# Kernel optimization log

Measured on AMD Instinct MI355X. Metric: run time of the kernel, lower is better.

The kernel has to match this reference:

```python
import jax, jax.numpy as jnp
import numpy as np


def squash(s, axis):
    # torch: mag_sq/(1+mag_sq) * s/mag, reduced over the given axis
    mag_sq = jnp.sum(s * s, axis=axis, keepdims=True)
    mag = jnp.sqrt(mag_sq)
    return mag_sq / (1.0 + mag_sq) * (s / mag)


def setup_inputs() -> dict:
    key = jax.random.key(0)
    ks = jax.random.split(key, 13)
    B, D_IN, H = 64, 227989, 512
    NU, CO, K = 8, 8, 8            # num_primary_units, conv out channels, kernel
    L = (H - K) // 2 + 1           # 253
    PSIZE = NU * 0 + CO * L        # 2024 per primary capsule
    NOUT, USIZE = 4, 64            # output capsules
    f32 = jnp.float32
    return {
        "x": jax.random.normal(ks[0], (B, D_IN), f32),
        "fc_w": jax.random.normal(ks[1], (H, D_IN), f32) * 0.002,
        "fc_b": jax.random.normal(ks[2], (H,), f32) * 0.01,
        "conv_w": jax.random.normal(ks[3], (NU, CO, 1, K), f32) * 0.1,
        "conv_b": jax.random.normal(ks[4], (NU, CO), f32) * 0.01,
        "W_dig": jax.random.normal(ks[5], (PSIZE, NOUT, USIZE, NU), f32) * 0.05,
        "fc2_w1": jax.random.normal(ks[6], (128, 256), f32) * 0.05,
        "fc2_b1": jnp.zeros((128,), f32),
        "fc2_w2": jax.random.normal(ks[7], (64, 128), f32) * 0.08,
        "fc2_b2": jnp.zeros((64,), f32),
        "fc2_w3": jax.random.normal(ks[8], (2, 64), f32) * 0.1,
        "fc2_b3": jnp.zeros((2,), f32),
    }


def reference(x, fc_w, fc_b, conv_w, conv_b, W_dig,
              fc2_w1, fc2_b1, fc2_w2, fc2_b2, fc2_w3, fc2_b3):
    B = x.shape[0]
    # fc + ReLU (nn.ReLU overwrote the LeakyReLU attribute)
    sdae = jnp.maximum(x @ fc_w.T + fc_b, 0.0)[:, None, :]   # [B,1,512]

    # primary capsules (no routing): 8 ConvUnits fused into one conv
    NU, CO, _, K = conv_w.shape
    rhs = conv_w.reshape(NU * CO, 1, K)
    u = jax.lax.conv_general_dilated(sdae, rhs, (2,), 'VALID',
                                     dimension_numbers=('NCH', 'OIH', 'NCH'))
    u = u + conv_b.reshape(1, NU * CO, 1)                     # [B,64,253]
    u = u.reshape(B, NU, -1)                                  # [B,8,2024]
    u = squash(u, 2)

    # digits capsule: dynamic routing, 3 iterations
    xt = jnp.swapaxes(u, 1, 2)                                # [B,2024,8]
    u_hat = jnp.einsum('cjdi,bci->bcjd', W_dig, xt)           # [B,2024,4,64]
    C, J = W_dig.shape[0], W_dig.shape[1]
    b_ij = jnp.zeros((C, J), u_hat.dtype)
    for _ in range(3):
        c_ij = jax.nn.softmax(b_ij, axis=0)                   # softmax over in_channels
        s_j = jnp.einsum('cj,bcjd->bjd', c_ij, u_hat)         # [B,4,64]
        v_j = squash(s_j, 1)                                  # torch squashes dim=2 = capsule dim j
        b_ij = b_ij + jnp.mean(jnp.einsum('bcjd,bjd->bcj', u_hat, v_j), axis=0)

    caps = v_j.reshape(B, -1)                                 # [B,256]
    lrelu = lambda z: jnp.where(z >= 0, z, 0.01 * z)          # LeakyReLU; dropout in eval = identity
    h = lrelu(caps @ fc2_w1.T + fc2_b1)
    h = lrelu(h @ fc2_w2.T + fc2_b2)
    logits = h @ fc2_w3.T + fc2_b3                            # [B,2]
    return (logits, sdae)
```

## Files before the change

kernel.cpp:

```cpp
#include <hip/hip_runtime.h>
#include <hip/hip_bf16.h>

typedef __attribute__((ext_vector_type(8))) short s16x8;
typedef __attribute__((ext_vector_type(4))) float f32x4;

#define D_IN 227989
#define KSPLIT 128
#define KC 1792
#define NSTEPS 28
#define RPITCH 68
#define BUFSZ (128 * RPITCH)

__device__ __forceinline__ s16x8 pk2(f32x4 lo, f32x4 hi) {
    union { int i[4]; s16x8 s; } u;
    asm("v_cvt_pk_bf16_f32 %0, %1, %2" : "=v"(u.i[0]) : "v"(lo[0]), "v"(lo[1]));
    asm("v_cvt_pk_bf16_f32 %0, %1, %2" : "=v"(u.i[1]) : "v"(lo[2]), "v"(lo[3]));
    asm("v_cvt_pk_bf16_f32 %0, %1, %2" : "=v"(u.i[2]) : "v"(hi[0]), "v"(hi[1]));
    asm("v_cvt_pk_bf16_f32 %0, %1, %2" : "=v"(u.i[3]) : "v"(hi[2]), "v"(hi[3]));
    return u.s;
}

__device__ __forceinline__ void gload_lds16(const float* g, float* l) {
    __builtin_amdgcn_global_load_lds(
        (const __attribute__((address_space(1))) void*)g,
        (__attribute__((address_space(3))) void*)l, 16, 0, 0);
}

__device__ __forceinline__ s16x8 sel8(const float* rowp, int pos0, bool b0, bool b1) {
    f32x4 i0 = *(const f32x4*)(rowp + pos0);
    f32x4 i1 = *(const f32x4*)(rowp + pos0 + 4);
    f32x4 i2 = *(const f32x4*)(rowp + pos0 + 8);
    float in[12] = {i0[0], i0[1], i0[2], i0[3], i1[0], i1[1], i1[2], i1[3],
                    i2[0], i2[1], i2[2], i2[3]};
    float tv[10];
    #pragma unroll
    for (int i = 0; i < 10; ++i) tv[i] = b0 ? in[i + 1] : in[i];
    f32x4 lo, hi;
    #pragma unroll
    for (int e = 0; e < 4; ++e) lo[e] = b1 ? tv[e + 2] : tv[e];
    #pragma unroll
    for (int e = 0; e < 4; ++e) hi[e] = b1 ? tv[e + 6] : tv[e + 4];
    return pk2(lo, hi);
}

__device__ __forceinline__ void compute_tile(const float* buf, int wid, int frow,
                                             int koct, bool b0, bool b1, f32x4* acc) {
    const float* B = buf + (64 + wid * 16 + frow) * RPITCH;
    const s16x8 bb0 = sel8(B, koct * 8, b0, b1);
    const s16x8 bb1 = sel8(B, 32 + koct * 8, b0, b1);
    #pragma unroll
    for (int m = 0; m < 4; ++m) {
        const float* A = buf + (m * 16 + frow) * RPITCH;
        const s16x8 a0 = sel8(A, koct * 8, b0, b1);
        const s16x8 a1 = sel8(A, 32 + koct * 8, b0, b1);
        acc[m] = __builtin_amdgcn_mfma_f32_16x16x32_bf16(a0, bb0, acc[m], 0, 0, 0);
        acc[m] = __builtin_amdgcn_mfma_f32_16x16x32_bf16(a1, bb1, acc[m], 0, 0, 0);
    }
}

__global__ __launch_bounds__(256) void k_fc_gemm(const float* __restrict__ x,
                                                 const float* __restrict__ w,
                                                 float* __restrict__ part) {
    __shared__ __align__(16) float lds[2 * BUFSZ];
    const int t = threadIdx.x;
    const int wid = t >> 6, lane = t & 63;
    const int frow = lane & 15, koct = lane >> 4;
    const int bx = blockIdx.x;
    const int nt = bx & 7, ks = bx >> 3;
    const long k0 = (long)ks * KC;
    const bool b0 = (frow & 1) != 0, b1 = (frow & 2) != 0;

    f32x4 acc[4] = {};

    if (ks < KSPLIT - 1) {
        const float* gp[9];
        int jdst[9];
        #pragma unroll
        for (int jj = 0; jj < 9; ++jj) {
            int j = jj * 4 + wid;
            if (j >= 34) j -= 34;
            jdst[jj] = j * 256;
            const int ch = j * 64 + lane;
            const int row = ch / 17;
            const int c = ch - row * 17;
            const float* base = (row < 64)
                ? (x + (long)row * D_IN)
                : (w + (long)(nt * 64 + (row - 64)) * D_IN);
            gp[jj] = base + (k0 - (row & 3)) + c * 4;
        }
        float* L0 = lds;
        float* L1 = lds + BUFSZ;

#define STAGE(BUF, OFF) do {                                   \
    _Pragma("unroll")                                          \
    for (int jj = 0; jj < 9; ++jj)                             \
        gload_lds16(gp[jj] + (OFF), (BUF) + jdst[jj]);         \
} while (0)

        STAGE(L0, 0);
        #pragma unroll 1
        for (int s = 0; s < NSTEPS; s += 2) {
            STAGE(L1, (s + 1) * 64);
            asm volatile("s_waitcnt vmcnt(9)" ::: "memory");
            __builtin_amdgcn_s_barrier();
            asm volatile("" ::: "memory");
            compute_tile(L0, wid, frow, koct, b0, b1, acc);
            asm volatile("s_waitcnt lgkmcnt(0)" ::: "memory");
            __builtin_amdgcn_s_barrier();
            if (s + 2 < NSTEPS) {
                STAGE(L0, (s + 2) * 64);
                asm volatile("s_waitcnt vmcnt(9)" ::: "memory");
            } else {
                asm volatile("s_waitcnt vmcnt(0)" ::: "memory");
            }
            __builtin_amdgcn_s_barrier();
            asm volatile("" ::: "memory");
            compute_tile(L1, wid, frow, koct, b0, b1, acc);
            asm volatile("s_waitcnt lgkmcnt(0)" ::: "memory");
            __builtin_amdgcn_s_barrier();
        }
#undef STAGE
    } else {
        const int rem = (int)(D_IN - k0);
        const int nst = (rem + 63) >> 6;
        const float* ga = x + (long)(wid * 16) * D_IN + k0 + lane;
        const float* gb = w + (long)(nt * 64 + wid * 16) * D_IN + k0 + lane;
        for (int s = 0; s < nst; ++s) {
            const int kk = s * 64 + lane;
            const bool ok = kk < rem;
            float va[16], vb[16];
            #pragma unroll
            for (int i = 0; i < 16; ++i) {
                va[i] = ok ? ga[(long)i * D_IN + s * 64] : 0.0f;
                vb[i] = ok ? gb[(long)i * D_IN + s * 64] : 0.0f;
            }
            __syncthreads();
            #pragma unroll
            for (int i = 0; i < 16; ++i) {
                lds[(wid * 16 + i) * RPITCH + lane] = va[i];
                lds[(64 + wid * 16 + i) * RPITCH + lane] = vb[i];
            }
            if (lane < 8) {
                const int rr = (lane & 3), half = lane >> 2;
                (void)rr; (void)half;
            }
            __syncthreads();
            compute_tile(lds, wid, frow, koct, false, false, acc);
            __syncthreads();
        }
    }

    const int g16 = nt * 4 + wid;
    float* __restrict__ po = part + ((long)(g16 * KSPLIT + ks) << 10);
    #pragma unroll
    for (int m = 0; m < 4; ++m)
        #pragma unroll
        for (int r = 0; r < 4; ++r)
            po[(m * 16 + koct * 4 + r) * 16 + frow] = acc[m][r];
}

__global__ __launch_bounds__(256) void k_fc_reduce(const float* __restrict__ part,
                                                   const float* __restrict__ bias,
                                                   float* __restrict__ sdae) {
    const int i = blockIdx.x * 256 + threadIdx.x;
    const int m = i >> 9, n = i & 511;
    const int nt = n >> 4, nl = n & 15;
    const float* p = part + ((long)nt * KSPLIT << 10) + m * 16 + nl;
    float s = 0.f;
    #pragma unroll 4
    for (int ks = 0; ks < KSPLIT; ++ks) s += p[(long)ks << 10];
    s += bias[n];
    sdae[i] = fmaxf(s, 0.0f);
}

__global__ __launch_bounds__(256) void k_conv_squash(const float* __restrict__ sdae,
                                                     const float* __restrict__ cw,
                                                     const float* __restrict__ cb,
                                                     float* __restrict__ xt) {
    __shared__ float row_s[512];
    __shared__ float us[64 * 253];
    __shared__ float part[256];
    __shared__ float scale_s[8];
    const int b = blockIdx.x, t = threadIdx.x;
    row_s[t] = sdae[b * 512 + t];
    row_s[t + 256] = sdae[b * 512 + t + 256];
    __syncthreads();
    const int ch = t >> 2, lq = t & 3;
    float wreg[8];
    #pragma unroll
    for (int k = 0; k < 8; ++k) wreg[k] = cw[ch * 8 + k];
    const float bias = cb[ch];
    const int l0 = lq * 64;
    const int l1 = (lq == 3) ? 253 : (l0 + 64);
    float ssq = 0.f;
    for (int l = l0; l < l1; ++l) {
        float v = bias;
        #pragma unroll
        for (int k = 0; k < 8; ++k) v += row_s[2 * l + k] * wreg[k];
        us[ch * 253 + l] = v;
        ssq += v * v;
    }
    part[t] = ssq;
    __syncthreads();
    if (t < 8) {
        float s = 0.f;
        for (int i = 0; i < 32; ++i) s += part[t * 32 + i];
        scale_s[t] = sqrtf(s) / (1.0f + s);
    }
    __syncthreads();
    const int nu = ch >> 3, co = ch & 7;
    const float sc = scale_s[nu];
    for (int l = l0; l < l1; ++l)
        xt[(long)b * 16192 + (long)(co * 253 + l) * 8 + nu] = us[ch * 253 + l] * sc;
}

template <int UNIFORM>
__global__ __launch_bounds__(256) void k_route_s(const float* __restrict__ W,
                                                 const float* __restrict__ xt,
                                                 const float* __restrict__ cij,
                                                 float* __restrict__ spart) {
    __shared__ __align__(16) float xs[64 * 132];
    __shared__ __align__(16) float wsh[16 * 768];
    const int bx = blockIdx.x;
    const int j = bx >> 6, cs = bx & 63;
    const int c0 = cs * 32;
    const int t = threadIdx.x;
    const int bg = t >> 4, dg = t & 15;
    float acc[4][4] = {};
    #pragma unroll 1
    for (int cc0 = 0; cc0 < 32; cc0 += 16) {
        {
            const int bb = t >> 2, p = t & 3;
            const float* src = xt + (long)bb * 16192 + (long)(c0 + cc0) * 8 + p * 32;
            float* dst = &xs[bb * 132 + p * 32];
            if (c0 + cc0 + 16 <= 2024) {
                #pragma unroll
                for (int e = 0; e < 32; e += 4) *(f32x4*)(dst + e) = *(const f32x4*)(src + e);
            } else {
                for (int e = 0; e < 32; ++e) {
                    int cidx = c0 + cc0 + ((p * 32 + e) >> 3);
                    dst[e] = (cidx < 2024) ? src[e] : 0.0f;
                }
            }
        }
        {
            const int ccs = t >> 4, dp = t & 15;
            const int c = c0 + cc0 + ccs;
            float* o = &wsh[ccs * 768 + dp * 48];
            if (c < 2024) {
                const float sc = UNIFORM ? (1.0f / 2024.0f) : cij[j * 2024 + c];
                const float* wsrc = W + (long)c * 2048 + j * 512 + dp * 32;
                #pragma unroll
                for (int dd = 0; dd < 4; ++dd) {
                    f32x4 w0 = *(const f32x4*)(wsrc + dd * 8);
                    f32x4 w1 = *(const f32x4*)(wsrc + dd * 8 + 4);
                    float* od = o + dd * 12;
                    od[0] = w0[0] * sc; od[1] = w0[1] * sc; od[2] = w0[2] * sc; od[3] = w0[3] * sc;
                    od[4] = w1[0] * sc; od[5] = w1[1] * sc; od[6] = w1[2] * sc; od[7] = w1[3] * sc;
                }
            } else {
                #pragma unroll
                for (int dd = 0; dd < 4; ++dd) {
                    float* od = o + dd * 12;
                    #pragma unroll
                    for (int e = 0; e < 8; ++e) od[e] = 0.0f;
                }
            }
        }
        __syncthreads();
        int ccN = 2024 - c0 - cc0;
        if (ccN > 16) ccN = 16;
        for (int cc = 0; cc < ccN; ++cc) {
            float xv[4][8], wv[4][8];
            #pragma unroll
            for (int bb = 0; bb < 4; ++bb) {
                *(f32x4*)&xv[bb][0] = *(const f32x4*)&xs[(bg * 4 + bb) * 132 + cc * 8];
                *(f32x4*)&xv[bb][4] = *(const f32x4*)&xs[(bg * 4 + bb) * 132 + cc * 8 + 4];
            }
            #pragma unroll
            for (int dd = 0; dd < 4; ++dd) {
                const int d = dg + dd * 16;
                *(f32x4*)&wv[dd][0] = *(const f32x4*)&wsh[cc * 768 + d * 12];
                *(f32x4*)&wv[dd][4] = *(const f32x4*)&wsh[cc * 768 + d * 12 + 4];
            }
            #pragma unroll
            for (int bb = 0; bb < 4; ++bb)
                #pragma unroll
                for (int dd = 0; dd < 4; ++dd)
                    #pragma unroll
                    for (int i = 0; i < 8; ++i)
                        acc[bb][dd] += xv[bb][i] * wv[dd][i];
        }
        __syncthreads();
    }
    float* sp = spart + ((long)bx << 12);
    #pragma unroll
    for (int bb = 0; bb < 4; ++bb)
        #pragma unroll
        for (int dd = 0; dd < 4; ++dd)
            sp[(bg * 4 + bb) * 64 + dg + dd * 16] = acc[bb][dd];
}

__global__ __launch_bounds__(256) void k_route_v(const float* __restrict__ spart,
                                                 float* __restrict__ v) {
    __shared__ float sj[256];
    const int b = blockIdx.x, t = threadIdx.x;
    const int d = t & 63;
    const int j = t >> 6;
    float s = 0.f;
    #pragma unroll 4
    for (int cs = 0; cs < 64; ++cs)
        s += spart[((long)(j * 64 + cs) << 12) + (b << 6) + d];
    sj[t] = s;
    __syncthreads();
    float msq = 0.f;
    #pragma unroll
    for (int q = 0; q < 4; ++q) { float z = sj[q * 64 + d]; msq += z * z; }
    v[(b << 8) + t] = s * (sqrtf(msq) / (1.0f + msq));
}

template <int ADD>
__global__ __launch_bounds__(256) void k_route_a(const float* __restrict__ W,
                                                 const float* __restrict__ xt,
                                                 const float* __restrict__ v,
                                                 float* __restrict__ bij) {
    __shared__ __align__(16) float xts[64 * 68];
    __shared__ __align__(16) float vts[4 * 4360];
    __shared__ float red[256];
    const int c0 = blockIdx.x * 8;
    const int t = threadIdx.x;
    for (int idx = t; idx < 16384; idx += 256) {
        int b = idx >> 8, r = idx & 255;
        vts[(r >> 6) * 4360 + (r & 63) * 68 + b] = v[idx];
    }
    for (int idx = t; idx < 4096; idx += 256) {
        int b = idx >> 6, r = idx & 63;
        xts[r * 68 + b] = xt[(long)b * 16192 + (long)c0 * 8 + r];
    }
    __syncthreads();
    const int cc = t >> 5, jj = (t >> 3) & 3, p = t & 7;
    float Wreg[8][8];
    const float* wb = W + (long)(c0 + cc) * 2048 + jj * 512;
    #pragma unroll
    for (int dd = 0; dd < 8; ++dd) {
        const int d = p + dd * 8;
        *(f32x4*)&Wreg[dd][0] = *(const f32x4*)(wb + d * 8);
        *(f32x4*)&Wreg[dd][4] = *(const f32x4*)(wb + d * 8 + 4);
    }
    float a0 = 0.f, a1 = 0.f, a2 = 0.f, a3 = 0.f;
    for (int b0 = 0; b0 < 64; b0 += 4) {
        float xq[8][4];
        #pragma unroll
        for (int i = 0; i < 8; ++i)
            *(f32x4*)&xq[i][0] = *(const f32x4*)&xts[(cc * 8 + i) * 68 + b0];
        #pragma unroll
        for (int dd = 0; dd < 8; ++dd) {
            const int d = p + dd * 8;
            f32x4 vq = *(const f32x4*)&vts[jj * 4360 + d * 68 + b0];
            float u0 = 0, u1 = 0, u2 = 0, u3 = 0;
            #pragma unroll
            for (int i = 0; i < 8; ++i) {
                const float wv = Wreg[dd][i];
                u0 += wv * xq[i][0]; u1 += wv * xq[i][1];
                u2 += wv * xq[i][2]; u3 += wv * xq[i][3];
            }
            a0 += u0 * vq[0]; a1 += u1 * vq[1]; a2 += u2 * vq[2]; a3 += u3 * vq[3];
        }
    }
    red[t] = a0 + a1 + a2 + a3;
    __syncthreads();
    if (p == 0) {
        float s = 0.f;
        #pragma unroll
        for (int q2 = 0; q2 < 8; ++q2) s += red[t + q2];
        s *= (1.0f / 64.0f);
        const int idx = (c0 + cc) * 4 + jj;
        bij[idx] = ADD ? (bij[idx] + s) : s;
    }
}

__global__ __launch_bounds__(256) void k_softmax(const float* __restrict__ bij,
                                                 float* __restrict__ cij) {
    __shared__ float red[256];
    const int j = blockIdx.x, t = threadIdx.x;
    float vals[8];
    float m = -1e30f;
    #pragma unroll
    for (int q = 0; q < 8; ++q) {
        const int c = q * 256 + t;
        const float z = (c < 2024) ? bij[c * 4 + j] : -1e30f;
        vals[q] = z;
        m = fmaxf(m, z);
    }
    red[t] = m;
    __syncthreads();
    for (int s = 128; s > 0; s >>= 1) {
        if (t < s) red[t] = fmaxf(red[t], red[t + s]);
        __syncthreads();
    }
    m = red[0];
    __syncthreads();
    float sum = 0.f;
    #pragma unroll
    for (int q = 0; q < 8; ++q) {
        const int c = q * 256 + t;
        const float e = (c < 2024) ? __expf(vals[q] - m) : 0.0f;
        vals[q] = e;
        sum += e;
    }
    red[t] = sum;
    __syncthreads();
    for (int s = 128; s > 0; s >>= 1) {
        if (t < s) red[t] += red[t + s];
        __syncthreads();
    }
    const float inv = 1.0f / red[0];
    #pragma unroll
    for (int q = 0; q < 8; ++q) {
        const int c = q * 256 + t;
        if (c < 2024) cij[j * 2024 + c] = vals[q] * inv;
    }
}

__global__ __launch_bounds__(256) void k_fc2(const float* __restrict__ v,
                                             const float* __restrict__ w1, const float* __restrict__ b1,
                                             const float* __restrict__ w2, const float* __restrict__ b2,
                                             const float* __restrict__ w3, const float* __restrict__ b3,
                                             float* __restrict__ logits) {
    __shared__ float caps[256], h1[128], h2[64];
    const int b = blockIdx.x, t = threadIdx.x;
    caps[t] = v[b * 256 + t];
    __syncthreads();
    if (t < 128) {
        float s = b1[t];
        const float* wr = w1 + t * 256;
        for (int k = 0; k < 256; ++k) s += wr[k] * caps[k];
        h1[t] = (s >= 0.f) ? s : 0.01f * s;
    }
    __syncthreads();
    if (t < 64) {
        float s = b2[t];
        const float* wr = w2 + t * 128;
        for (int k = 0; k < 128; ++k) s += wr[k] * h1[k];
        h2[t] = (s >= 0.f) ? s : 0.01f * s;
    }
    __syncthreads();
    if (t < 2) {
        float s = b3[t];
        const float* wr = w3 + t * 64;
        for (int k = 0; k < 64; ++k) s += wr[k] * h2[k];
        logits[b * 2 + t] = s;
    }
}

extern "C" void kernel_launch(void* const* d_in, const int* in_sizes, int n_in,
                              void* d_out, int out_size, void* d_ws, size_t ws_size,
                              hipStream_t stream) {
    const float* x      = (const float*)d_in[0];
    const float* fc_w   = (const float*)d_in[1];
    const float* fc_b   = (const float*)d_in[2];
    const float* conv_w = (const float*)d_in[3];
    const float* conv_b = (const float*)d_in[4];
    const float* W_dig  = (const float*)d_in[5];
    const float* w1 = (const float*)d_in[6];
    const float* b1 = (const float*)d_in[7];
    const float* w2 = (const float*)d_in[8];
    const float* b2 = (const float*)d_in[9];
    const float* w3 = (const float*)d_in[10];
    const float* b3 = (const float*)d_in[11];

    float* out    = (float*)d_out;
    float* logits = out;
    float* sdae   = out + 128;

    float* ws     = (float*)d_ws;
    float* ws_fc  = ws;
    float* ws_xt  = ws_fc + 4194304;
    float* ws_sp  = ws_xt + 1036288;
    float* ws_v   = ws_sp + 1048576;
    float* ws_bij = ws_v + 16384;
    float* ws_cij = ws_bij + 8096;

    k_fc_gemm<<<1024, 256, 0, stream>>>(x, fc_w, ws_fc);
    k_fc_reduce<<<128, 256, 0, stream>>>(ws_fc, fc_b, sdae);
    k_conv_squash<<<64, 256, 0, stream>>>(sdae, conv_w, conv_b, ws_xt);

    k_route_s<1><<<256, 256, 0, stream>>>(W_dig, ws_xt, ws_cij, ws_sp);
    k_route_v<<<64, 256, 0, stream>>>(ws_sp, ws_v);
    k_route_a<0><<<253, 256, 0, stream>>>(W_dig, ws_xt, ws_v, ws_bij);
    k_softmax<<<4, 256, 0, stream>>>(ws_bij, ws_cij);
    k_route_s<0><<<256, 256, 0, stream>>>(W_dig, ws_xt, ws_cij, ws_sp);
    k_route_v<<<64, 256, 0, stream>>>(ws_sp, ws_v);
    k_route_a<1><<<253, 256, 0, stream>>>(W_dig, ws_xt, ws_v, ws_bij);
    k_softmax<<<4, 256, 0, stream>>>(ws_bij, ws_cij);
    k_route_s<0><<<256, 256, 0, stream>>>(W_dig, ws_xt, ws_cij, ws_sp);
    k_route_v<<<64, 256, 0, stream>>>(ws_sp, ws_v);

    k_fc2<<<64, 256, 0, stream>>>(ws_v, w1, b1, w2, b2, w3, b3, logits);
}
```

Before: 305.2 us.

## Double GEMM K-step per stage and fuse reduce/conv, softmax and final route kernels

The FC GEMM now stages 128 K-columns per LDS buffer instead of 64, halving the number of steps and barriers at the cost of twice the LDS footprint. The split-K reduction is fused into the conv+squash kernel, the softmax kernels are folded into route_s (each block recomputes the softmax reduction), and the last route_v is fused with the fc2 MLP. This removes four to five kernel launches and the c_ij round trip through memory, in exchange for redundant softmax work in every route_s block and lower occupancy in the GEMM from the larger shared buffers.

```diff
diff --git a/kernel.cpp b/kernel.cpp
--- a/kernel.cpp
+++ b/kernel.cpp
@@ -7,8 +7,8 @@
 #define D_IN 227989
 #define KSPLIT 128
 #define KC 1792
-#define NSTEPS 28
-#define RPITCH 68
+#define NSTEPS 14
+#define RPITCH 132
 #define BUFSZ (128 * RPITCH)
 
 __device__ __forceinline__ s16x8 pk2(f32x4 lo, f32x4 hi) {
@@ -43,18 +43,19 @@
     return pk2(lo, hi);
 }
 
-__device__ __forceinline__ void compute_tile(const float* buf, int wid, int frow,
-                                             int koct, bool b0, bool b1, f32x4* acc) {
+__device__ __forceinline__ void compute_tile128(const float* buf, int wid, int frow,
+                                                int koct, bool b0, bool b1, f32x4* acc) {
     const float* B = buf + (64 + wid * 16 + frow) * RPITCH;
-    const s16x8 bb0 = sel8(B, koct * 8, b0, b1);
-    const s16x8 bb1 = sel8(B, 32 + koct * 8, b0, b1);
-    #pragma unroll
-    for (int m = 0; m < 4; ++m) {
-        const float* A = buf + (m * 16 + frow) * RPITCH;
-        const s16x8 a0 = sel8(A, koct * 8, b0, b1);
-        const s16x8 a1 = sel8(A, 32 + koct * 8, b0, b1);
-        acc[m] = __builtin_amdgcn_mfma_f32_16x16x32_bf16(a0, bb0, acc[m], 0, 0, 0);
-        acc[m] = __builtin_amdgcn_mfma_f32_16x16x32_bf16(a1, bb1, acc[m], 0, 0, 0);
+    #pragma unroll
+    for (int kk = 0; kk < 4; ++kk) {
+        const int pos0 = kk * 32 + koct * 8;
+        const s16x8 bb = sel8(B, pos0, b0, b1);
+        #pragma unroll
+        for (int m = 0; m < 4; ++m) {
+            const float* A = buf + (m * 16 + frow) * RPITCH;
+            const s16x8 aa = sel8(A, pos0, b0, b1);
+            acc[m] = __builtin_amdgcn_mfma_f32_16x16x32_bf16(aa, bb, acc[m], 0, 0, 0);
+        }
     }
 }
 
@@ -73,49 +74,48 @@
     f32x4 acc[4] = {};
 
     if (ks < KSPLIT - 1) {
-        const float* gp[9];
-        int jdst[9];
-        #pragma unroll
-        for (int jj = 0; jj < 9; ++jj) {
-            int j = jj * 4 + wid;
-            if (j >= 34) j -= 34;
-            jdst[jj] = j * 256;
-            const int ch = j * 64 + lane;
-            const int row = ch / 17;
-            const int c = ch - row * 17;
+        const int wbase = (wid == 0) ? 0 : (wid == 1) ? 1088 : (wid == 2) ? 2176 : 3136;
+        const float* gp[17];
+        int jdst[17];
+        #pragma unroll
+        for (int jj = 0; jj < 17; ++jj) {
+            const int ch = wbase + jj * 64 + lane;
+            const int row = ch / 33;
+            const int c = ch - row * 33;
             const float* base = (row < 64)
                 ? (x + (long)row * D_IN)
                 : (w + (long)(nt * 64 + (row - 64)) * D_IN);
             gp[jj] = base + (k0 - (row & 3)) + c * 4;
+            jdst[jj] = (wbase + jj * 64) * 4;
         }
         float* L0 = lds;
         float* L1 = lds + BUFSZ;
 
 #define STAGE(BUF, OFF) do {                                   \
     _Pragma("unroll")                                          \
-    for (int jj = 0; jj < 9; ++jj)                             \
+    for (int jj = 0; jj < 17; ++jj)                            \
         gload_lds16(gp[jj] + (OFF), (BUF) + jdst[jj]);         \
 } while (0)
 
         STAGE(L0, 0);
         #pragma unroll 1
         for (int s = 0; s < NSTEPS; s += 2) {
-            STAGE(L1, (s + 1) * 64);
-            asm volatile("s_waitcnt vmcnt(9)" ::: "memory");
+            STAGE(L1, (s + 1) * 128);
+            asm volatile("s_waitcnt vmcnt(17)" ::: "memory");
             __builtin_amdgcn_s_barrier();
             asm volatile("" ::: "memory");
-            compute_tile(L0, wid, frow, koct, b0, b1, acc);
+            compute_tile128(L0, wid, frow, koct, b0, b1, acc);
             asm volatile("s_waitcnt lgkmcnt(0)" ::: "memory");
             __builtin_amdgcn_s_barrier();
             if (s + 2 < NSTEPS) {
-                STAGE(L0, (s + 2) * 64);
-                asm volatile("s_waitcnt vmcnt(9)" ::: "memory");
+                STAGE(L0, (s + 2) * 128);
+                asm volatile("s_waitcnt vmcnt(17)" ::: "memory");
             } else {
                 asm volatile("s_waitcnt vmcnt(0)" ::: "memory");
             }
             __builtin_amdgcn_s_barrier();
             asm volatile("" ::: "memory");
-            compute_tile(L1, wid, frow, koct, b0, b1, acc);
+            compute_tile128(L1, wid, frow, koct, b0, b1, acc);
             asm volatile("s_waitcnt lgkmcnt(0)" ::: "memory");
             __builtin_amdgcn_s_barrier();
         }
@@ -140,12 +140,19 @@
                 lds[(wid * 16 + i) * RPITCH + lane] = va[i];
                 lds[(64 + wid * 16 + i) * RPITCH + lane] = vb[i];
             }
-            if (lane < 8) {
-                const int rr = (lane & 3), half = lane >> 2;
-                (void)rr; (void)half;
-            }
             __syncthreads();
-            compute_tile(lds, wid, frow, koct, false, false, acc);
+            const float* B = lds + (64 + wid * 16 + frow) * RPITCH;
+            #pragma unroll
+            for (int q = 0; q < 2; ++q) {
+                const int pos0 = q * 32 + koct * 8;
+                const s16x8 bb = sel8(B, pos0, false, false);
+                #pragma unroll
+                for (int m = 0; m < 4; ++m) {
+                    const float* A = lds + (m * 16 + frow) * RPITCH;
+                    const s16x8 aa = sel8(A, pos0, false, false);
+                    acc[m] = __builtin_amdgcn_mfma_f32_16x16x32_bf16(aa, bb, acc[m], 0, 0, 0);
+                }
+            }
             __syncthreads();
         }
     }
@@ -159,31 +166,30 @@
             po[(m * 16 + koct * 4 + r) * 16 + frow] = acc[m][r];
 }
 
-__global__ __launch_bounds__(256) void k_fc_reduce(const float* __restrict__ part,
-                                                   const float* __restrict__ bias,
-                                                   float* __restrict__ sdae) {
-    const int i = blockIdx.x * 256 + threadIdx.x;
-    const int m = i >> 9, n = i & 511;
-    const int nt = n >> 4, nl = n & 15;
-    const float* p = part + ((long)nt * KSPLIT << 10) + m * 16 + nl;
-    float s = 0.f;
-    #pragma unroll 4
-    for (int ks = 0; ks < KSPLIT; ++ks) s += p[(long)ks << 10];
-    s += bias[n];
-    sdae[i] = fmaxf(s, 0.0f);
-}
-
-__global__ __launch_bounds__(256) void k_conv_squash(const float* __restrict__ sdae,
+__global__ __launch_bounds__(256) void k_reduce_conv(const float* __restrict__ part,
+                                                     const float* __restrict__ fc_b,
                                                      const float* __restrict__ cw,
                                                      const float* __restrict__ cb,
+                                                     float* __restrict__ sdae,
                                                      float* __restrict__ xt) {
     __shared__ float row_s[512];
     __shared__ float us[64 * 253];
-    __shared__ float part[256];
+    __shared__ float psum[256];
     __shared__ float scale_s[8];
     const int b = blockIdx.x, t = threadIdx.x;
-    row_s[t] = sdae[b * 512 + t];
-    row_s[t + 256] = sdae[b * 512 + t + 256];
+    #pragma unroll
+    for (int h = 0; h < 2; ++h) {
+        const int n = t + h * 256;
+        const int g16 = n >> 4, nl = n & 15;
+        const float* p = part + ((long)(g16 * KSPLIT) << 10) + b * 16 + nl;
+        float s = 0.f;
+        #pragma unroll 4
+        for (int ks = 0; ks < KSPLIT; ++ks) s += p[(long)ks << 10];
+        s += fc_b[n];
+        s = fmaxf(s, 0.0f);
+        row_s[n] = s;
+        sdae[b * 512 + n] = s;
+    }
     __syncthreads();
     const int ch = t >> 2, lq = t & 3;
     float wreg[8];
@@ -200,11 +206,11 @@
         us[ch * 253 + l] = v;
         ssq += v * v;
     }
-    part[t] = ssq;
+    psum[t] = ssq;
     __syncthreads();
     if (t < 8) {
         float s = 0.f;
-        for (int i = 0; i < 32; ++i) s += part[t * 32 + i];
+        for (int i = 0; i < 32; ++i) s += psum[t * 32 + i];
         scale_s[t] = sqrtf(s) / (1.0f + s);
     }
     __syncthreads();
@@ -214,18 +220,54 @@
         xt[(long)b * 16192 + (long)(co * 253 + l) * 8 + nu] = us[ch * 253 + l] * sc;
 }
 
-template <int UNIFORM>
+template <int SM>
 __global__ __launch_bounds__(256) void k_route_s(const float* __restrict__ W,
                                                  const float* __restrict__ xt,
-                                                 const float* __restrict__ cij,
+                                                 const float* __restrict__ bij,
                                                  float* __restrict__ spart) {
     __shared__ __align__(16) float xs[64 * 132];
     __shared__ __align__(16) float wsh[16 * 768];
+    __shared__ float red[256];
     const int bx = blockIdx.x;
     const int j = bx >> 6, cs = bx & 63;
     const int c0 = cs * 32;
     const int t = threadIdx.x;
     const int bg = t >> 4, dg = t & 15;
+
+    float Mx = 0.f, Sx = 0.f;
+    if (SM) {
+        float vals[8];
+        float m = -1e30f;
+        #pragma unroll
+        for (int q = 0; q < 8; ++q) {
+            const int c = q * 256 + t;
+            const float z = (c < 2024) ? bij[c * 4 + j] : -1e30f;
+            vals[q] = z;
+            m = fmaxf(m, z);
+        }
+        red[t] = m;
+        __syncthreads();
+        for (int s2 = 128; s2 > 0; s2 >>= 1) {
+            if (t < s2) red[t] = fmaxf(red[t], red[t + s2]);
+            __syncthreads();
+        }
+        Mx = red[0];
+        __syncthreads();
+        float sum = 0.f;
+        #pragma unroll
+        for (int q = 0; q < 8; ++q) {
+            const int c = q * 256 + t;
+            sum += (c < 2024) ? __expf(vals[q] - Mx) : 0.0f;
+        }
+        red[t] = sum;
+        __syncthreads();
+        for (int s2 = 128; s2 > 0; s2 >>= 1) {
+            if (t < s2) red[t] += red[t + s2];
+            __syncthreads();
+        }
+        Sx = 1.0f / red[0];
+    }
+
     float acc[4][4] = {};
     #pragma unroll 1
     for (int cc0 = 0; cc0 < 32; cc0 += 16) {
@@ -248,7 +290,8 @@
             const int c = c0 + cc0 + ccs;
             float* o = &wsh[ccs * 768 + dp * 48];
             if (c < 2024) {
-                const float sc = UNIFORM ? (1.0f / 2024.0f) : cij[j * 2024 + c];
+                const float sc = SM ? (__expf(bij[c * 4 + j] - Mx) * Sx)
+                                    : (1.0f / 2024.0f);
                 const float* wsrc = W + (long)c * 2048 + j * 512 + dp * 32;
                 #pragma unroll
                 for (int dd = 0; dd < 4; ++dd) {
@@ -379,77 +422,46 @@
     }
 }
 
-__global__ __launch_bounds__(256) void k_softmax(const float* __restrict__ bij,
-                                                 float* __restrict__ cij) {
-    __shared__ float red[256];
-    const int j = blockIdx.x, t = threadIdx.x;
-    float vals[8];
-    float m = -1e30f;
-    #pragma unroll
-    for (int q = 0; q < 8; ++q) {
-        const int c = q * 256 + t;
-        const float z = (c < 2024) ? bij[c * 4 + j] : -1e30f;
-        vals[q] = z;
-        m = fmaxf(m, z);
-    }
-    red[t] = m;
-    __syncthreads();
-    for (int s = 128; s > 0; s >>= 1) {
-        if (t < s) red[t] = fmaxf(red[t], red[t + s]);
-        __syncthreads();
-    }
-    m = red[0];
-    __syncthreads();
-    float sum = 0.f;
-    #pragma unroll
-    for (int q = 0; q < 8; ++q) {
-        const int c = q * 256 + t;
-        const float e = (c < 2024) ? __expf(vals[q] - m) : 0.0f;
-        vals[q] = e;
-        sum += e;
-    }
-    red[t] = sum;
-    __syncthreads();
-    for (int s = 128; s > 0; s >>= 1) {
-        if (t < s) red[t] += red[t + s];
-        __syncthreads();
-    }
-    const float inv = 1.0f / red[0];
-    #pragma unroll
-    for (int q = 0; q < 8; ++q) {
-        const int c = q * 256 + t;
-        if (c < 2024) cij[j * 2024 + c] = vals[q] * inv;
-    }
-}
-
-__global__ __launch_bounds__(256) void k_fc2(const float* __restrict__ v,
-                                             const float* __restrict__ w1, const float* __restrict__ b1,
-                                             const float* __restrict__ w2, const float* __restrict__ b2,
-                                             const float* __restrict__ w3, const float* __restrict__ b3,
-                                             float* __restrict__ logits) {
+__global__ __launch_bounds__(256) void k_route_v_fc2(const float* __restrict__ spart,
+                                                     const float* __restrict__ w1, const float* __restrict__ b1,
+                                                     const float* __restrict__ w2, const float* __restrict__ b2,
+                                                     const float* __restrict__ w3, const float* __restrict__ b3,
+                                                     float* __restrict__ logits) {
+    __shared__ float sj[256];
     __shared__ float caps[256], h1[128], h2[64];
     const int b = blockIdx.x, t = threadIdx.x;
-    caps[t] = v[b * 256 + t];
+    const int d = t & 63;
+    const int j = t >> 6;
+    float s = 0.f;
+    #pragma unroll 4
+    for (int cs = 0; cs < 64; ++cs)
+        s += spart[((long)(j * 64 + cs) << 12) + (b << 6) + d];
+    sj[t] = s;
+    __syncthreads();
+    float msq = 0.f;
+    #pragma unroll
+    for (int q = 0; q < 4; ++q) { float z = sj[q * 64 + d]; msq += z * z; }
+    caps[t] = s * (sqrtf(msq) / (1.0f + msq));
     __syncthreads();
     if (t < 128) {
-        float s = b1[t];
+        float acc = b1[t];
         const float* wr = w1 + t * 256;
-        for (int k = 0; k < 256; ++k) s += wr[k] * caps[k];
-        h1[t] = (s >= 0.f) ? s : 0.01f * s;
+        for (int k = 0; k < 256; ++k) acc += wr[k] * caps[k];
+        h1[t] = (acc >= 0.f) ? acc : 0.01f * acc;
     }
     __syncthreads();
     if (t < 64) {
-        float s = b2[t];
+        float acc = b2[t];
         const float* wr = w2 + t * 128;
-        for (int k = 0; k < 128; ++k) s += wr[k] * h1[k];
-        h2[t] = (s >= 0.f) ? s : 0.01f * s;
+        for (int k = 0; k < 128; ++k) acc += wr[k] * h1[k];
+        h2[t] = (acc >= 0.f) ? acc : 0.01f * acc;
     }
     __syncthreads();
     if (t < 2) {
-        float s = b3[t];
+        float acc = b3[t];
         const float* wr = w3 + t * 64;
-        for (int k = 0; k < 64; ++k) s += wr[k] * h2[k];
-        logits[b * 2 + t] = s;
+        for (int k = 0; k < 64; ++k) acc += wr[k] * h2[k];
+        logits[b * 2 + t] = acc;
     }
 }
 
@@ -479,22 +491,16 @@
     float* ws_sp  = ws_xt + 1036288;
     float* ws_v   = ws_sp + 1048576;
     float* ws_bij = ws_v + 16384;
-    float* ws_cij = ws_bij + 8096;
 
     k_fc_gemm<<<1024, 256, 0, stream>>>(x, fc_w, ws_fc);
-    k_fc_reduce<<<128, 256, 0, stream>>>(ws_fc, fc_b, sdae);
-    k_conv_squash<<<64, 256, 0, stream>>>(sdae, conv_w, conv_b, ws_xt);
-
-    k_route_s<1><<<256, 256, 0, stream>>>(W_dig, ws_xt, ws_cij, ws_sp);
+    k_reduce_conv<<<64, 256, 0, stream>>>(ws_fc, fc_b, conv_w, conv_b, sdae, ws_xt);
+
+    k_route_s<0><<<256, 256, 0, stream>>>(W_dig, ws_xt, ws_bij, ws_sp);
     k_route_v<<<64, 256, 0, stream>>>(ws_sp, ws_v);
     k_route_a<0><<<253, 256, 0, stream>>>(W_dig, ws_xt, ws_v, ws_bij);
-    k_softmax<<<4, 256, 0, stream>>>(ws_bij, ws_cij);
-    k_route_s<0><<<256, 256, 0, stream>>>(W_dig, ws_xt, ws_cij, ws_sp);
+    k_route_s<1><<<256, 256, 0, stream>>>(W_dig, ws_xt, ws_bij, ws_sp);
     k_route_v<<<64, 256, 0, stream>>>(ws_sp, ws_v);
     k_route_a<1><<<253, 256, 0, stream>>>(W_dig, ws_xt, ws_v, ws_bij);
-    k_softmax<<<4, 256, 0, stream>>>(ws_bij, ws_cij);
-    k_route_s<0><<<256, 256, 0, stream>>>(W_dig, ws_xt, ws_cij, ws_sp);
-    k_route_v<<<64, 256, 0, stream>>>(ws_sp, ws_v);
-
-    k_fc2<<<64, 256, 0, stream>>>(ws_v, w1, b1, w2, b2, w3, b3, logits);
-}
+    k_route_s<1><<<256, 256, 0, stream>>>(W_dig, ws_xt, ws_bij, ws_sp);
+    k_route_v_fc2<<<64, 256, 0, stream>>>(ws_sp, w1, b1, w2, b2, w3, b3, logits);
+}
```

New measurement: 338.9 us. 1.11x slower.
